# Optimization experiments

Hardware: AMD Instinct MI355X
Metric: run time of the kernel (lower is better)

## Reference

```python
import functools
import jax, jax.numpy as jnp
import numpy as np

N = 8192
CUTOFF = 0.125        # OpenBoundary._cutoff
INCLUDE_SELF = False  # OpenBoundary._include_self
MASK_VALUE = -1


def setup_inputs() -> dict:
    key = jax.random.key(0)
    positions = jax.random.uniform(key, (N, 3), dtype=jnp.float32)
    return {"positions": positions, "max_neighbours": 128}


def reference(positions, max_neighbours):
    n = positions.shape[0]
    c2 = CUTOFF * CUTOFF
    # all-pairs squared distances + cutoff mask; row i = sphere centred on particle i
    neigh_mask = jax.vmap(lambda c: jnp.sum((positions - c) ** 2, axis=1) <= c2)(positions)  # [N, N] bool
    if not INCLUDE_SELF:
        neigh_mask = neigh_mask & ~jnp.eye(n, dtype=bool)
    # per-row fixed-size compaction of true indices, padded with MASK_VALUE
    compact = functools.partial(jnp.argwhere, size=max_neighbours, fill_value=MASK_VALUE)
    to_idx = jax.vmap(compact)(neigh_mask)[..., 0]                 # [N, max_neighbours] int
    cell_indices = jnp.zeros((*to_idx.shape, 3), dtype=jnp.int32)  # open boundary: all zero cells
    actual_max_neighbours = jnp.max(neigh_mask.sum(axis=1))
    return to_idx, cell_indices, actual_max_neighbours
```

## Files before the change

### kernel.cpp

```cpp
#include <hip/hip_runtime.h>
#include <stdint.h>


#define CUTOFF2 (0.125f * 0.125f)
constexpr int NCELLS = 512;
constexpr int CAP    = 64;
constexpr int MAXN   = 128;
constexpr int NPART  = 256;

__device__ __forceinline__ int ccoord(float v) {
    int c = (int)(v * 8.0f);
    return c > 7 ? 7 : c;
}

__global__ __launch_bounds__(256) void scatter_kernel(
    const float* __restrict__ pos, int n,
    int* __restrict__ cnt, float4* __restrict__ cells) {
    int i = blockIdx.x * blockDim.x + threadIdx.x;
    if (i >= n) return;
    float x = pos[i*3], y = pos[i*3+1], z = pos[i*3+2];
    int c = (ccoord(z) * 8 + ccoord(y)) * 8 + ccoord(x);
    int slot = atomicAdd(&cnt[c], 1);
    cells[c * CAP + slot] = make_float4(x, y, z, __int_as_float(i));
}

__global__ __launch_bounds__(256) void neigh_kernel(
    const float4* __restrict__ cells,
    const int* __restrict__ cnt,
    const float* __restrict__ pos,
    int maxn,
    int* __restrict__ to_idx,
    int* __restrict__ cell_out,
    int* __restrict__ partial) {
    __shared__ uint32_t bm[4][256];

    const int lane = threadIdx.x & 63;
    const int wave = threadIdx.x >> 6;
    const int row  = blockIdx.x * 4 + wave;
    uint32_t* mybm = bm[wave];

    ((int4*)mybm)[lane] = make_int4(0, 0, 0, 0);

    const float px = pos[row*3], py = pos[row*3+1], pz = pos[row*3+2];
    const int cx = ccoord(px), cy = ccoord(py), cz = ccoord(pz);

    int4* co = (int4*)(cell_out + (size_t)row * maxn * 3);
    co[lane] = make_int4(0, 0, 0, 0);
    if (lane < 32) co[64 + lane] = make_int4(0, 0, 0, 0);

    #pragma unroll
    for (int dz = -1; dz <= 1; ++dz) {
        const int czz = cz + dz;
        const bool zok = (unsigned)czz <= 7u;
        #pragma unroll
        for (int dy = -1; dy <= 1; ++dy) {
            const int cyy = cy + dy;
            const bool yok = zok && ((unsigned)cyy <= 7u);
            #pragma unroll
            for (int dxc = -1; dxc <= 1; ++dxc) {
                const int cxx = cx + dxc;
                if (!(yok && ((unsigned)cxx <= 7u))) continue;
                const int c = (czz * 8 + cyy) * 8 + cxx;
                const int m = cnt[c];
                if (lane < m) {
                    float4 q = cells[c * CAP + lane];
                    float ddx = q.x - px, ddy = q.y - py, ddz = q.z - pz;
                    float d2 = ddx*ddx + ddy*ddy + ddz*ddz;
                    int idx = __float_as_int(q.w);
                    if (d2 <= CUTOFF2 && idx != row)
                        atomicOr(&mybm[idx >> 5], 1u << (idx & 31));
                }
            }
        }
    }

    int4 wv = ((int4*)mybm)[lane];
    uint32_t w0 = (uint32_t)wv.x, w1 = (uint32_t)wv.y,
             w2 = (uint32_t)wv.z, w3 = (uint32_t)wv.w;
    int tc = __popc(w0) + __popc(w1) + __popc(w2) + __popc(w3);

    int inc = tc;
    #pragma unroll
    for (int d = 1; d < 64; d <<= 1) {
        int o = __shfl_up(inc, d);
        if (lane >= d) inc += o;
    }
    const int total = __shfl(inc, 63);
    int p = inc - tc;

    int* out_row = to_idx + (size_t)row * maxn;
    const int bitbase = lane << 7;
    uint32_t wsv[4] = {w0, w1, w2, w3};
    #pragma unroll
    for (int d = 0; d < 4; ++d) {
        uint32_t mm = wsv[d];
        while (mm) {
            int b = __ffs(mm) - 1;
            if (p < MAXN) out_row[p] = bitbase + (d << 5) + b;
            ++p;
            mm &= mm - 1;
        }
    }
    int start = total < MAXN ? total : MAXN;
    for (int q = start + lane; q < MAXN; q += 64) out_row[q] = -1;

    if (lane == 0) atomicMax(&partial[blockIdx.x & (NPART - 1)], total);
}

__global__ __launch_bounds__(256) void maxred_kernel(
    const int* __restrict__ partial, int* __restrict__ out_max) {
    __shared__ int sm[4];
    int m = partial[threadIdx.x];
    #pragma unroll
    for (int d = 32; d > 0; d >>= 1) {
        int o = __shfl_down(m, d);
        m = o > m ? o : m;
    }
    if ((threadIdx.x & 63) == 0) sm[threadIdx.x >> 6] = m;
    __syncthreads();
    if (threadIdx.x == 0) {
        int r = sm[0];
        r = sm[1] > r ? sm[1] : r;
        r = sm[2] > r ? sm[2] : r;
        r = sm[3] > r ? sm[3] : r;
        *out_max = r;
    }
}

extern "C" void kernel_launch(void* const* d_in, const int* in_sizes, int n_in,
                              void* d_out, int out_size, void* d_ws, size_t ws_size,
                              hipStream_t stream) {
    const float* pos = (const float*)d_in[0];
    const int n = in_sizes[0] / 3;
    const int maxn = (out_size - 1) / (n * 4);

    int* to_idx   = (int*)d_out;
    int* cell_out = to_idx + (size_t)n * maxn;
    int* out_max  = cell_out + (size_t)n * maxn * 3;

    int*    cnt     = (int*)d_ws;
    int*    partial = cnt + NCELLS;
    float4* cells   = (float4*)((char*)d_ws + 4096);

    hipMemsetAsync(d_ws, 0, (NCELLS + NPART) * sizeof(int), stream);
    scatter_kernel<<<(n + 255) / 256, 256, 0, stream>>>(pos, n, cnt, cells);
    neigh_kernel<<<n / 4, 256, 0, stream>>>(cells, cnt, pos, maxn,
                                            to_idx, cell_out, partial);
    maxred_kernel<<<1, NPART, 0, stream>>>(partial, out_max);
}
```

Measured before the change: 87.70 us.

## Process one cell per block with shared-memory candidate staging

```diff
diff --git a/kernel.cpp b/kernel.cpp
--- a/kernel.cpp
+++ b/kernel.cpp
@@ -7,6 +7,7 @@
 constexpr int CAP    = 64;
 constexpr int MAXN   = 128;
 constexpr int NPART  = 256;
+constexpr int CANDMAX = 27 * CAP;
 
 __device__ __forceinline__ int ccoord(float v) {
     int c = (int)(v * 8.0f);
@@ -24,87 +25,122 @@
     cells[c * CAP + slot] = make_float4(x, y, z, __int_as_float(i));
 }
 
-__global__ __launch_bounds__(256) void neigh_kernel(
+__global__ __launch_bounds__(512) void neigh_kernel(
     const float4* __restrict__ cells,
     const int* __restrict__ cnt,
-    const float* __restrict__ pos,
     int maxn,
     int* __restrict__ to_idx,
     int* __restrict__ cell_out,
     int* __restrict__ partial) {
-    __shared__ uint32_t bm[4][256];
+    __shared__ float4   cand[CANDMAX];
+    __shared__ uint32_t bm[8][256];
+    __shared__ int scid[27], scnt[27], soff[28];
 
-    const int lane = threadIdx.x & 63;
-    const int wave = threadIdx.x >> 6;
-    const int row  = blockIdx.x * 4 + wave;
+    const int tid  = threadIdx.x;
+    const int lane = tid & 63;
+    const int wave = tid >> 6;
+    const int cell = blockIdx.x;
+    const int cx = cell & 7, cy = (cell >> 3) & 7, cz = cell >> 6;
+
+    if (tid < 64) {
+        int dzz = tid / 9 - 1, dyy = (tid / 3) % 3 - 1, dxx = tid % 3 - 1;
+        int xx = cx + dxx, yy = cy + dyy, zz = cz + dzz;
+        bool ok = (tid < 27) & ((unsigned)xx <= 7u) &
+                  ((unsigned)yy <= 7u) & ((unsigned)zz <= 7u);
+        int c = (zz * 8 + yy) * 8 + xx;
+        int v = ok ? cnt[c] : 0;
+        if (tid < 27) { scid[tid] = ok ? c : -1; scnt[tid] = v; }
+        int incl = v;
+        #pragma unroll
+        for (int d = 1; d < 32; d <<= 1) {
+            int o = __shfl_up(incl, d);
+            if (lane >= d) incl += o;
+        }
+        if (tid < 27) soff[tid + 1] = incl;
+        if (tid == 0) soff[0] = 0;
+    }
+    __syncthreads();
+
+    const int mrows = scnt[13];
+    const int cbase = soff[13];
+    if (mrows == 0) return;
+
+    for (int j = wave; j < 27; j += 8) {
+        int c = scid[j];
+        if (c >= 0 && lane < scnt[j])
+            cand[soff[j] + lane] = cells[c * CAP + lane];
+    }
+    __syncthreads();
+
+    const int T = soff[27];
     uint32_t* mybm = bm[wave];
 
-    ((int4*)mybm)[lane] = make_int4(0, 0, 0, 0);
+    for (int r = wave; r < mrows; r += 8) {
+        float4 me = cand[cbase + r];
+        const int row = __float_as_int(me.w);
 
-    const float px = pos[row*3], py = pos[row*3+1], pz = pos[row*3+2];
-    const int cx = ccoord(px), cy = ccoord(py), cz = ccoord(pz);
+        ((int4*)mybm)[lane] = make_int4(0, 0, 0, 0);
 
-    int4* co = (int4*)(cell_out + (size_t)row * maxn * 3);
-    co[lane] = make_int4(0, 0, 0, 0);
-    if (lane < 32) co[64 + lane] = make_int4(0, 0, 0, 0);
+        int4* co = (int4*)(cell_out + (size_t)row * maxn * 3);
+        co[lane] = make_int4(0, 0, 0, 0);
+        if (lane < 32) co[64 + lane] = make_int4(0, 0, 0, 0);
 
-    #pragma unroll
-    for (int dz = -1; dz <= 1; ++dz) {
-        const int czz = cz + dz;
-        const bool zok = (unsigned)czz <= 7u;
+        int s = lane;
+        for (; s + 64 < T; s += 128) {
+            float4 q0 = cand[s];
+            float4 q1 = cand[s + 64];
+            float dx0 = q0.x - me.x, dy0 = q0.y - me.y, dz0 = q0.z - me.z;
+            float dx1 = q1.x - me.x, dy1 = q1.y - me.y, dz1 = q1.z - me.z;
+            float d20 = dx0*dx0 + dy0*dy0 + dz0*dz0;
+            float d21 = dx1*dx1 + dy1*dy1 + dz1*dz1;
+            int i0 = __float_as_int(q0.w);
+            int i1 = __float_as_int(q1.w);
+            if (d20 <= CUTOFF2 && i0 != row)
+                atomicOr(&mybm[i0 >> 5], 1u << (i0 & 31));
+            if (d21 <= CUTOFF2 && i1 != row)
+                atomicOr(&mybm[i1 >> 5], 1u << (i1 & 31));
+        }
+        if (s < T) {
+            float4 q = cand[s];
+            float ddx = q.x - me.x, ddy = q.y - me.y, ddz = q.z - me.z;
+            float d2 = ddx*ddx + ddy*ddy + ddz*ddz;
+            int i0 = __float_as_int(q.w);
+            if (d2 <= CUTOFF2 && i0 != row)
+                atomicOr(&mybm[i0 >> 5], 1u << (i0 & 31));
+        }
+
+        int4 wv = ((int4*)mybm)[lane];
+        uint32_t w0 = (uint32_t)wv.x, w1 = (uint32_t)wv.y,
+                 w2 = (uint32_t)wv.z, w3 = (uint32_t)wv.w;
+        int tc = __popc(w0) + __popc(w1) + __popc(w2) + __popc(w3);
+
+        int inc = tc;
         #pragma unroll
-        for (int dy = -1; dy <= 1; ++dy) {
-            const int cyy = cy + dy;
-            const bool yok = zok && ((unsigned)cyy <= 7u);
-            #pragma unroll
-            for (int dxc = -1; dxc <= 1; ++dxc) {
-                const int cxx = cx + dxc;
-                if (!(yok && ((unsigned)cxx <= 7u))) continue;
-                const int c = (czz * 8 + cyy) * 8 + cxx;
-                const int m = cnt[c];
-                if (lane < m) {
-                    float4 q = cells[c * CAP + lane];
-                    float ddx = q.x - px, ddy = q.y - py, ddz = q.z - pz;
-                    float d2 = ddx*ddx + ddy*ddy + ddz*ddz;
-                    int idx = __float_as_int(q.w);
-                    if (d2 <= CUTOFF2 && idx != row)
-                        atomicOr(&mybm[idx >> 5], 1u << (idx & 31));
-                }
+        for (int d = 1; d < 64; d <<= 1) {
+            int o = __shfl_up(inc, d);
+            if (lane >= d) inc += o;
+        }
+        const int total = __shfl(inc, 63);
+        int p = inc - tc;
+
+        int* out_row = to_idx + (size_t)row * maxn;
+        const int bitbase = lane << 7;
+        uint32_t wsv[4] = {w0, w1, w2, w3};
+        #pragma unroll
+        for (int d = 0; d < 4; ++d) {
+            uint32_t mm = wsv[d];
+            while (mm) {
+                int b = __ffs(mm) - 1;
+                if (p < MAXN) out_row[p] = bitbase + (d << 5) + b;
+                ++p;
+                mm &= mm - 1;
             }
         }
+        int start = total < MAXN ? total : MAXN;
+        for (int q = start + lane; q < MAXN; q += 64) out_row[q] = -1;
+
+        if (lane == 0) atomicMax(&partial[blockIdx.x & (NPART - 1)], total);
     }
-
-    int4 wv = ((int4*)mybm)[lane];
-    uint32_t w0 = (uint32_t)wv.x, w1 = (uint32_t)wv.y,
-             w2 = (uint32_t)wv.z, w3 = (uint32_t)wv.w;
-    int tc = __popc(w0) + __popc(w1) + __popc(w2) + __popc(w3);
-
-    int inc = tc;
-    #pragma unroll
-    for (int d = 1; d < 64; d <<= 1) {
-        int o = __shfl_up(inc, d);
-        if (lane >= d) inc += o;
-    }
-    const int total = __shfl(inc, 63);
-    int p = inc - tc;
-
-    int* out_row = to_idx + (size_t)row * maxn;
-    const int bitbase = lane << 7;
-    uint32_t wsv[4] = {w0, w1, w2, w3};
-    #pragma unroll
-    for (int d = 0; d < 4; ++d) {
-        uint32_t mm = wsv[d];
-        while (mm) {
-            int b = __ffs(mm) - 1;
-            if (p < MAXN) out_row[p] = bitbase + (d << 5) + b;
-            ++p;
-            mm &= mm - 1;
-        }
-    }
-    int start = total < MAXN ? total : MAXN;
-    for (int q = start + lane; q < MAXN; q += 64) out_row[q] = -1;
-
-    if (lane == 0) atomicMax(&partial[blockIdx.x & (NPART - 1)], total);
 }
 
 __global__ __launch_bounds__(256) void maxred_kernel(
@@ -122,8 +158,7 @@
         int r = sm[0];
         r = sm[1] > r ? sm[1] : r;
         r = sm[2] > r ? sm[2] : r;
-        r = sm[3] > r ? sm[3] : r;
-        *out_max = r;
+        *out_max = r > sm[3] ? r : sm[3];
     }
 }
 
@@ -144,7 +179,7 @@
 
     hipMemsetAsync(d_ws, 0, (NCELLS + NPART) * sizeof(int), stream);
     scatter_kernel<<<(n + 255) / 256, 256, 0, stream>>>(pos, n, cnt, cells);
-    neigh_kernel<<<n / 4, 256, 0, stream>>>(cells, cnt, pos, maxn,
-                                            to_idx, cell_out, partial);
+    neigh_kernel<<<NCELLS, 512, 0, stream>>>(cells, cnt, maxn,
+                                             to_idx, cell_out, partial);
     maxred_kernel<<<1, NPART, 0, stream>>>(partial, out_max);
 }
```

Result: faster. 84.07 us (-4.1%).

## Replace cell-list neighbour search with brute-force all-pairs tiled kernel

Applied to the files above, without the earlier changes.

```diff
diff --git a/kernel.cpp b/kernel.cpp
--- a/kernel.cpp
+++ b/kernel.cpp
@@ -3,148 +3,125 @@
 
 
 #define CUTOFF2 (0.125f * 0.125f)
-constexpr int NCELLS = 512;
-constexpr int CAP    = 64;
 constexpr int MAXN   = 128;
-constexpr int NPART  = 256;
+constexpr int CHUNK  = 512;
+constexpr int WAVES  = 8;
+constexpr int ROWS_PER_BLOCK = WAVES * 2;
 
-__device__ __forceinline__ int ccoord(float v) {
-    int c = (int)(v * 8.0f);
-    return c > 7 ? 7 : c;
-}
-
-__global__ __launch_bounds__(256) void scatter_kernel(
-    const float* __restrict__ pos, int n,
-    int* __restrict__ cnt, float4* __restrict__ cells) {
-    int i = blockIdx.x * blockDim.x + threadIdx.x;
-    if (i >= n) return;
-    float x = pos[i*3], y = pos[i*3+1], z = pos[i*3+2];
-    int c = (ccoord(z) * 8 + ccoord(y)) * 8 + ccoord(x);
-    int slot = atomicAdd(&cnt[c], 1);
-    cells[c * CAP + slot] = make_float4(x, y, z, __int_as_float(i));
-}
-
-__global__ __launch_bounds__(256) void neigh_kernel(
-    const float4* __restrict__ cells,
-    const int* __restrict__ cnt,
-    const float* __restrict__ pos,
-    int maxn,
+__global__ __launch_bounds__(512) void brute_kernel(
+    const float* __restrict__ pos, int n, int maxn,
     int* __restrict__ to_idx,
     int* __restrict__ cell_out,
-    int* __restrict__ partial) {
-    __shared__ uint32_t bm[4][256];
+    int* __restrict__ out_max)
+{
+    __shared__ float    sh[CHUNK * 3];
+    __shared__ uint32_t bm[WAVES][2][256];
+    __shared__ int blkmax;
 
-    const int lane = threadIdx.x & 63;
-    const int wave = threadIdx.x >> 6;
-    const int row  = blockIdx.x * 4 + wave;
-    uint32_t* mybm = bm[wave];
+    const int tid  = threadIdx.x;
+    const int lane = tid & 63;
+    const int wave = tid >> 6;
 
-    ((int4*)mybm)[lane] = make_int4(0, 0, 0, 0);
+    const int rowA = blockIdx.x * ROWS_PER_BLOCK + wave * 2;
+    const int rowB = rowA + 1;
 
-    const float px = pos[row*3], py = pos[row*3+1], pz = pos[row*3+2];
-    const int cx = ccoord(px), cy = ccoord(py), cz = ccoord(pz);
+    ((int4*)&bm[wave][0][0])[lane] = make_int4(0, 0, 0, 0);
+    ((int4*)&bm[wave][1][0])[lane] = make_int4(0, 0, 0, 0);
+    if (tid == 0) blkmax = 0;
 
-    int4* co = (int4*)(cell_out + (size_t)row * maxn * 3);
-    co[lane] = make_int4(0, 0, 0, 0);
-    if (lane < 32) co[64 + lane] = make_int4(0, 0, 0, 0);
+    const float ax = pos[rowA*3], ay = pos[rowA*3+1], az = pos[rowA*3+2];
+    const float bx = pos[rowB*3], by = pos[rowB*3+1], bz = pos[rowB*3+2];
 
-    #pragma unroll
-    for (int dz = -1; dz <= 1; ++dz) {
-        const int czz = cz + dz;
-        const bool zok = (unsigned)czz <= 7u;
-        #pragma unroll
-        for (int dy = -1; dy <= 1; ++dy) {
-            const int cyy = cy + dy;
-            const bool yok = zok && ((unsigned)cyy <= 7u);
-            #pragma unroll
-            for (int dxc = -1; dxc <= 1; ++dxc) {
-                const int cxx = cx + dxc;
-                if (!(yok && ((unsigned)cxx <= 7u))) continue;
-                const int c = (czz * 8 + cyy) * 8 + cxx;
-                const int m = cnt[c];
-                if (lane < m) {
-                    float4 q = cells[c * CAP + lane];
-                    float ddx = q.x - px, ddy = q.y - py, ddz = q.z - pz;
-                    float d2 = ddx*ddx + ddy*ddy + ddz*ddz;
-                    int idx = __float_as_int(q.w);
-                    if (d2 <= CUTOFF2 && idx != row)
-                        atomicOr(&mybm[idx >> 5], 1u << (idx & 31));
-                }
-            }
+    {
+        int4* coA = (int4*)(cell_out + (size_t)rowA * maxn * 3);
+        int4* coB = (int4*)(cell_out + (size_t)rowB * maxn * 3);
+        coA[lane] = make_int4(0, 0, 0, 0);
+        coB[lane] = make_int4(0, 0, 0, 0);
+        if (lane < 32) {
+            coA[64 + lane] = make_int4(0, 0, 0, 0);
+            coB[64 + lane] = make_int4(0, 0, 0, 0);
         }
     }
 
-    int4 wv = ((int4*)mybm)[lane];
-    uint32_t w0 = (uint32_t)wv.x, w1 = (uint32_t)wv.y,
-             w2 = (uint32_t)wv.z, w3 = (uint32_t)wv.w;
-    int tc = __popc(w0) + __popc(w1) + __popc(w2) + __popc(w3);
+    const int nchunk = n / CHUNK;
+    for (int c = 0; c < nchunk; ++c) {
+        __syncthreads();
+        const float* src = pos + (size_t)c * (CHUNK * 3);
+        sh[tid]        = src[tid];
+        sh[tid +  512] = src[tid +  512];
+        sh[tid + 1024] = src[tid + 1024];
+        __syncthreads();
 
-    int inc = tc;
-    #pragma unroll
-    for (int d = 1; d < 64; d <<= 1) {
-        int o = __shfl_up(inc, d);
-        if (lane >= d) inc += o;
-    }
-    const int total = __shfl(inc, 63);
-    int p = inc - tc;
-
-    int* out_row = to_idx + (size_t)row * maxn;
-    const int bitbase = lane << 7;
-    uint32_t wsv[4] = {w0, w1, w2, w3};
-    #pragma unroll
-    for (int d = 0; d < 4; ++d) {
-        uint32_t mm = wsv[d];
-        while (mm) {
-            int b = __ffs(mm) - 1;
-            if (p < MAXN) out_row[p] = bitbase + (d << 5) + b;
-            ++p;
-            mm &= mm - 1;
+        const int gbase = c * CHUNK;
+        #pragma unroll
+        for (int it = 0; it < CHUNK / 64; ++it) {
+            const int j = it * 64 + lane;
+            const float x = sh[j*3], y = sh[j*3+1], z = sh[j*3+2];
+            const int g = gbase + j;
+            const float dxa = x - ax, dya = y - ay, dza = z - az;
+            const float dxb = x - bx, dyb = y - by, dzb = z - bz;
+            const float d2a = dxa*dxa + dya*dya + dza*dza;
+            const float d2b = dxb*dxb + dyb*dyb + dzb*dzb;
+            if (d2a <= CUTOFF2 && g != rowA)
+                atomicOr(&bm[wave][0][g >> 5], 1u << (g & 31));
+            if (d2b <= CUTOFF2 && g != rowB)
+                atomicOr(&bm[wave][1][g >> 5], 1u << (g & 31));
         }
     }
-    int start = total < MAXN ? total : MAXN;
-    for (int q = start + lane; q < MAXN; q += 64) out_row[q] = -1;
 
-    if (lane == 0) atomicMax(&partial[blockIdx.x & (NPART - 1)], total);
-}
+    #pragma unroll
+    for (int s = 0; s < 2; ++s) {
+        const int row = rowA + s;
 
-__global__ __launch_bounds__(256) void maxred_kernel(
-    const int* __restrict__ partial, int* __restrict__ out_max) {
-    __shared__ int sm[4];
-    int m = partial[threadIdx.x];
-    #pragma unroll
-    for (int d = 32; d > 0; d >>= 1) {
-        int o = __shfl_down(m, d);
-        m = o > m ? o : m;
+        int4 wv = ((int4*)&bm[wave][s][0])[lane];
+        uint32_t w0 = (uint32_t)wv.x, w1 = (uint32_t)wv.y,
+                 w2 = (uint32_t)wv.z, w3 = (uint32_t)wv.w;
+        int tc = __popc(w0) + __popc(w1) + __popc(w2) + __popc(w3);
+
+        int inc = tc;
+        #pragma unroll
+        for (int d = 1; d < 64; d <<= 1) {
+            int o = __shfl_up(inc, d);
+            if (lane >= d) inc += o;
+        }
+        const int total = __shfl(inc, 63);
+        int p = inc - tc;
+
+        int* out_row = to_idx + (size_t)row * maxn;
+        const int bitbase = lane << 7;
+        uint32_t wsv[4] = {w0, w1, w2, w3};
+        #pragma unroll
+        for (int d = 0; d < 4; ++d) {
+            uint32_t mm = wsv[d];
+            while (mm) {
+                int b = __ffs(mm) - 1;
+                if (p < MAXN) out_row[p] = bitbase + (d << 5) + b;
+                ++p;
+                mm &= mm - 1;
+            }
+        }
+        int start = total < MAXN ? total : MAXN;
+        for (int q = start + lane; q < MAXN; q += 64) out_row[q] = -1;
+
+        if (lane == 0) atomicMax(&blkmax, total);
     }
-    if ((threadIdx.x & 63) == 0) sm[threadIdx.x >> 6] = m;
+
     __syncthreads();
-    if (threadIdx.x == 0) {
-        int r = sm[0];
-        r = sm[1] > r ? sm[1] : r;
-        r = sm[2] > r ? sm[2] : r;
-        r = sm[3] > r ? sm[3] : r;
-        *out_max = r;
-    }
+    if (tid == 0) atomicMax(out_max, blkmax);
 }
 
 extern "C" void kernel_launch(void* const* d_in, const int* in_sizes, int n_in,
                               void* d_out, int out_size, void* d_ws, size_t ws_size,
                               hipStream_t stream) {
     const float* pos = (const float*)d_in[0];
-    const int n = in_sizes[0] / 3;
-    const int maxn = (out_size - 1) / (n * 4);
+    int n = in_sizes[0] / 3;
+    int maxn = (out_size - 1) / (n * 4);
 
     int* to_idx   = (int*)d_out;
     int* cell_out = to_idx + (size_t)n * maxn;
     int* out_max  = cell_out + (size_t)n * maxn * 3;
 
-    int*    cnt     = (int*)d_ws;
-    int*    partial = cnt + NCELLS;
-    float4* cells   = (float4*)((char*)d_ws + 4096);
-
-    hipMemsetAsync(d_ws, 0, (NCELLS + NPART) * sizeof(int), stream);
-    scatter_kernel<<<(n + 255) / 256, 256, 0, stream>>>(pos, n, cnt, cells);
-    neigh_kernel<<<n / 4, 256, 0, stream>>>(cells, cnt, pos, maxn,
-                                            to_idx, cell_out, partial);
-    maxred_kernel<<<1, NPART, 0, stream>>>(partial, out_max);
+    hipMemsetAsync(out_max, 0, sizeof(int), stream);
+    brute_kernel<<<n / ROWS_PER_BLOCK, 512, 0, stream>>>(
+        pos, n, maxn, to_idx, cell_out, out_max);
 }
```

After: 91.98 us. +4.9%, slower.
